# Optimization experiments

Hardware: AMD Instinct MI355X
Metric: run time of the kernel (lower is better)

Reference implementation:

```python
import jax, jax.numpy as jnp
import numpy as np

PD_THR = 1e-6  # positive-definiteness floor for the diagonal covariance

N_IN, DIM, BATCH = 8192, 128, 4096


def setup_inputs() -> dict:
    key = jax.random.key(0)
    kx, km = jax.random.split(key)
    x = jax.random.normal(kx, (BATCH, DIM), dtype=jnp.float32)
    mean = jax.random.normal(km, (N_IN, DIM), dtype=jnp.float32)
    diag = jnp.ones((N_IN, DIM), dtype=jnp.float32)
    return {"x": x, "mean": mean, "diag": diag}


def reference(x, mean, diag):
    """Energies[b, i] = KL( N(x_b, I) || N(mean_i, diag(diag_i)) ).

    Diagonal-Gaussian KL:
      0.5 * sum_d [ log(diag_id) + (1 + (x_bd - mu_id)^2) / diag_id - 1 ]

    The pairwise quadratic term is expanded into GEMMs to avoid the
    (batch, n_in, dim) broadcast intermediate:
      sum_d (x-mu)^2/diag = x^2 @ inv.T - 2 x @ (mu*inv).T + sum(mu^2*inv)
    Returns (batch, n_in), i.e. the original's energies.T.
    """
    d = jnp.clip(diag, PD_THR, None)              # (n_in, dim)
    inv = 1.0 / d                                 # (n_in, dim)
    # pairwise Mahalanobis quadratic, shape (batch, n_in)
    quad = (
        (x * x) @ inv.T
        - 2.0 * (x @ (mean * inv).T)
        + jnp.sum(mean * mean * inv, axis=-1)     # (n_in,) broadcast
    )
    # per-codebook constants: logdet + trace(inv) - dim
    const = jnp.sum(jnp.log(d), axis=-1) + jnp.sum(inv, axis=-1) - x.shape[-1]
    return 0.5 * (quad + const)                   # (batch, n_in)
```

## Files before the change

### kernel.cpp

```cpp
#include <hip/hip_runtime.h>
#include <hip/hip_bf16.h>


#define BATCH 4096
#define N_IN  8192
#define DIM   128
#define KPA   512
#define KPB   256
#define PD_THR 1e-6f

#define BM 256
#define BN 256
#define BK 64
#define NT (KPA / BK)

typedef __attribute__((ext_vector_type(4))) float f32x4;
typedef __attribute__((ext_vector_type(8))) short bf16x8;

static __device__ __forceinline__ unsigned short f2bf(float v) {
    union { __hip_bfloat16 h; unsigned short u; } cv;
    cv.h = __float2bfloat16(v);
    return cv.u;
}
static __device__ __forceinline__ float bf2f(unsigned short u) {
    union { unsigned short u; __hip_bfloat16 h; } cv;
    cv.u = u;
    return __bfloat162float(cv.h);
}

__global__ void prep_a_kernel(const float* __restrict__ x,
                              unsigned short* __restrict__ Ap) {
    int t = blockIdx.x * 256 + threadIdx.x;
    int row = t >> 7;
    int d   = t & 127;
    float v  = x[t];
    float x2 = v * v;
    unsigned short x2h = f2bf(x2);
    unsigned short x2l = f2bf(x2 - bf2f(x2h));
    unsigned short xh  = f2bf(v);
    unsigned short xl  = f2bf(v - bf2f(xh));
    unsigned short* a = Ap + (size_t)row * KPA;
    a[d]       = x2h;  a[128 + d] = xh;
    a[256 + d] = x2l;  a[384 + d] = xl;
}

__global__ void prep_b_kernel(const float* __restrict__ mean,
                              const float* __restrict__ diag,
                              unsigned short* __restrict__ Bp,
                              float* __restrict__ cvec) {
    int wave = threadIdx.x >> 6, lane = threadIdx.x & 63;
    int row = blockIdx.x * 4 + wave;
    const float* mrow = mean + (size_t)row * DIM;
    const float* drow = diag + (size_t)row * DIM;
    unsigned short* b = Bp + (size_t)row * KPB;
    float csum = 0.0f;
#pragma unroll
    for (int j = 0; j < 2; ++j) {
        int d = lane + 64 * j;
        float m   = mrow[d];
        float dd  = fmaxf(drow[d], PD_THR);
        float inv = 1.0f / dd;
        float fm  = -2.0f * m * inv;
        csum += m * m * inv + logf(dd) + inv;
        b[d]       = f2bf(inv);
        b[128 + d] = f2bf(fm);
    }
#pragma unroll
    for (int off = 32; off > 0; off >>= 1) csum += __shfl_down(csum, off);
    if (lane == 0) cvec[row] = csum - (float)DIM;
}

__global__ void __launch_bounds__(512, 2)
kl_gemm(const unsigned short* __restrict__ Ap,
        const unsigned short* __restrict__ Bp,
        const float* __restrict__ cvec,
        float* __restrict__ out) {
    __shared__ __align__(16) unsigned short lds[2][2 * BM * BK];

    int bid0 = blockIdx.x;
    int xcd = bid0 & 7, g = bid0 >> 3;
    int bx = (xcd & 1) * 8 + (g & 7);
    int by = (xcd >> 1) * 8 + (g >> 3);
    int m0 = bx * BM, n0 = by * BN;

    int tid  = threadIdx.x;
    int wave = tid >> 6, lane = tid & 63;
    int wr = wave >> 2, wc = wave & 3;

    const int lrow  = lane >> 3;
    const int lslot = (lane & 7) ^ lrow;

    const unsigned short* gA = Ap + (size_t)(m0 + wave * 8 + lrow) * KPA + lslot * 8;
    const unsigned short* gB = Bp + (size_t)(n0 + wave * 8 + lrow) * KPB + lslot * 8;

    f32x4 acc[8][4];
#pragma unroll
    for (int m = 0; m < 8; ++m)
#pragma unroll
        for (int n = 0; n < 4; ++n) acc[m][n] = (f32x4){0.f, 0.f, 0.f, 0.f};

    auto STAGE = [&](int b, int t) {
        int k0a = t * BK;
        int k0b = (t & 3) * BK;
#pragma unroll
        for (int j = 0; j < 4; ++j)
            __builtin_amdgcn_global_load_lds(
                (const __attribute__((address_space(1))) void*)(gA + (size_t)j * 64 * KPA + k0a),
                (__attribute__((address_space(3))) void*)&lds[b][(wave * 8 + j * 64) * 64],
                16, 0, 0);
#pragma unroll
        for (int j = 0; j < 4; ++j)
            __builtin_amdgcn_global_load_lds(
                (const __attribute__((address_space(1))) void*)(gB + (size_t)j * 64 * KPB + k0b),
                (__attribute__((address_space(3))) void*)&lds[b][16384 + (wave * 8 + j * 64) * 64],
                16, 0, 0);
    };

    auto COMPUTE = [&](int b) {
        const unsigned short* La = &lds[b][0];
        const unsigned short* Lb = &lds[b][16384];
#pragma unroll
        for (int kk = 0; kk < BK; kk += 32) {
            const int phys = ((((kk >> 3) + (lane >> 4))) ^ (lane & 7)) * 8;
            bf16x8 af[8], bf[4];
#pragma unroll
            for (int m = 0; m < 8; ++m)
                af[m] = *(const bf16x8*)&La[(wr * 128 + m * 16 + (lane & 15)) * 64 + phys];
#pragma unroll
            for (int n = 0; n < 4; ++n)
                bf[n] = *(const bf16x8*)&Lb[(wc * 64 + n * 16 + (lane & 15)) * 64 + phys];
            __builtin_amdgcn_s_setprio(1);
#pragma unroll
            for (int m = 0; m < 8; ++m)
#pragma unroll
                for (int n = 0; n < 4; ++n)
                    acc[m][n] = __builtin_amdgcn_mfma_f32_16x16x32_bf16(
                        af[m], bf[n], acc[m][n], 0, 0, 0);
            __builtin_amdgcn_s_setprio(0);
        }
    };

    STAGE(0, 0);
    STAGE(1, 1);
#pragma unroll 1
    for (int t = 0; t < NT - 1; ++t) {
        asm volatile("s_waitcnt vmcnt(8)" ::: "memory");
        __builtin_amdgcn_s_barrier();
        __builtin_amdgcn_sched_barrier(0);
        COMPUTE(t & 1);
        __builtin_amdgcn_s_barrier();
        __builtin_amdgcn_sched_barrier(0);
        if (t + 2 < NT) STAGE(t & 1, t + 2);
    }
    asm volatile("s_waitcnt vmcnt(0)" ::: "memory");
    __builtin_amdgcn_s_barrier();
    __builtin_amdgcn_sched_barrier(0);
    COMPUTE((NT - 1) & 1);
    __builtin_amdgcn_s_barrier();
    __builtin_amdgcn_sched_barrier(0);

    float* lbw = (float*)&lds[0][0] + wave * 1024;
    const int crow0 = m0 + wr * 128;
    const int ccol0 = n0 + wc * 64;
    const int lr = (lane >> 4) << 2;
    const int lc = lane & 15;
#pragma unroll
    for (int m = 0; m < 8; ++m) {
#pragma unroll
        for (int n = 0; n < 4; ++n)
#pragma unroll
            for (int r = 0; r < 4; ++r)
                lbw[(lr + r) * 64 + n * 16 + lc] = acc[m][n][r];
#pragma unroll
        for (int q = 0; q < 4; ++q) {
            int flat = q * 256 + lane * 4;
            int row  = flat >> 6;
            int col  = flat & 63;
            f32x4 v  = *(const f32x4*)&lbw[flat];
            f32x4 c4 = *(const f32x4*)&cvec[ccol0 + col];
            f32x4 o  = (v + c4) * 0.5f;
            __builtin_nontemporal_store(
                o, (f32x4*)&out[(size_t)(crow0 + m * 16 + row) * N_IN + ccol0 + col]);
        }
    }
}

extern "C" void kernel_launch(void* const* d_in, const int* in_sizes, int n_in_args,
                              void* d_out, int out_size, void* d_ws, size_t ws_size,
                              hipStream_t stream) {
    (void)in_sizes; (void)n_in_args; (void)out_size; (void)ws_size;
    const float* x    = (const float*)d_in[0];
    const float* mean = (const float*)d_in[1];
    const float* diag = (const float*)d_in[2];
    float* out = (float*)d_out;

    char* ws = (char*)d_ws;
    unsigned short* Bp = (unsigned short*)ws;
    unsigned short* Ap = (unsigned short*)(ws + (size_t)N_IN * KPB * 2);
    float* cvec = (float*)(ws + (size_t)N_IN * KPB * 2 + (size_t)BATCH * KPA * 2);

    prep_a_kernel<<<BATCH * DIM / 256, 256, 0, stream>>>(x, Ap);
    prep_b_kernel<<<N_IN / 4, 256, 0, stream>>>(mean, diag, Bp, cvec);
    kl_gemm<<<(BATCH / BM) * (N_IN / BN), 512, 0, stream>>>(Ap, Bp, cvec, out);
}
```

Before: 188.9 us.

## Shrink GEMM N tile to 128 and use triple-buffered LDS pipeline

Halves the block N tile from 256 to 128, so each wave computes a 64x64 sub-tile (4x4 MFMA accumulators instead of 8x4). LDS goes from two buffers to three, with loads issued three k-steps ahead and stepped vmcnt waits. The block-to-XCD mapping is reworked for the new 16x64 grid. This cuts register pressure and hides more global-load latency, but lowers arithmetic intensity per block and increases A-tile reloads across blocks.

```diff
diff --git a/kernel.cpp b/kernel.cpp
--- a/kernel.cpp
+++ b/kernel.cpp
@@ -10,9 +10,10 @@
 #define PD_THR 1e-6f
 
 #define BM 256
-#define BN 256
+#define BN 128
 #define BK 64
 #define NT (KPA / BK)
+#define BUFE (BM * BK + BN * BK)
 
 typedef __attribute__((ext_vector_type(4))) float f32x4;
 typedef __attribute__((ext_vector_type(8))) short bf16x8;
@@ -75,63 +76,64 @@
         const unsigned short* __restrict__ Bp,
         const float* __restrict__ cvec,
         float* __restrict__ out) {
-    __shared__ __align__(16) unsigned short lds[2][2 * BM * BK];
+    __shared__ __align__(16) unsigned short lds[3 * BUFE];
 
     int bid0 = blockIdx.x;
     int xcd = bid0 & 7, g = bid0 >> 3;
-    int bx = (xcd & 1) * 8 + (g & 7);
-    int by = (xcd >> 1) * 8 + (g >> 3);
+    int bx = (xcd & 3) * 4 + (g & 3);
+    int by = (xcd >> 2) * 32 + (g >> 2);
     int m0 = bx * BM, n0 = by * BN;
 
     int tid  = threadIdx.x;
     int wave = tid >> 6, lane = tid & 63;
-    int wr = wave >> 2, wc = wave & 3;
+    int wr = wave >> 1, wc = wave & 1;
 
     const int lrow  = lane >> 3;
     const int lslot = (lane & 7) ^ lrow;
 
     const unsigned short* gA = Ap + (size_t)(m0 + wave * 8 + lrow) * KPA + lslot * 8;
-    const unsigned short* gB = Bp + (size_t)(n0 + wave * 8 + lrow) * KPB + lslot * 8;
-
-    f32x4 acc[8][4];
-#pragma unroll
-    for (int m = 0; m < 8; ++m)
+    const unsigned short* gB = Bp + (size_t)(n0 + wave * 16 + lrow) * KPB + lslot * 8;
+
+    f32x4 acc[4][4];
+#pragma unroll
+    for (int m = 0; m < 4; ++m)
 #pragma unroll
         for (int n = 0; n < 4; ++n) acc[m][n] = (f32x4){0.f, 0.f, 0.f, 0.f};
 
     auto STAGE = [&](int b, int t) {
         int k0a = t * BK;
         int k0b = (t & 3) * BK;
+        unsigned short* base = &lds[b * BUFE];
 #pragma unroll
         for (int j = 0; j < 4; ++j)
             __builtin_amdgcn_global_load_lds(
                 (const __attribute__((address_space(1))) void*)(gA + (size_t)j * 64 * KPA + k0a),
-                (__attribute__((address_space(3))) void*)&lds[b][(wave * 8 + j * 64) * 64],
+                (__attribute__((address_space(3))) void*)&base[(wave * 8 + j * 64) * 64],
                 16, 0, 0);
 #pragma unroll
-        for (int j = 0; j < 4; ++j)
+        for (int j = 0; j < 2; ++j)
             __builtin_amdgcn_global_load_lds(
-                (const __attribute__((address_space(1))) void*)(gB + (size_t)j * 64 * KPB + k0b),
-                (__attribute__((address_space(3))) void*)&lds[b][16384 + (wave * 8 + j * 64) * 64],
+                (const __attribute__((address_space(1))) void*)(gB + (size_t)j * 8 * KPB + k0b),
+                (__attribute__((address_space(3))) void*)&base[BM * BK + (wave * 16 + j * 8) * 64],
                 16, 0, 0);
     };
 
     auto COMPUTE = [&](int b) {
-        const unsigned short* La = &lds[b][0];
-        const unsigned short* Lb = &lds[b][16384];
+        const unsigned short* La = &lds[b * BUFE];
+        const unsigned short* Lb = &lds[b * BUFE + BM * BK];
 #pragma unroll
         for (int kk = 0; kk < BK; kk += 32) {
-            const int phys = ((((kk >> 3) + (lane >> 4))) ^ (lane & 7)) * 8;
-            bf16x8 af[8], bf[4];
-#pragma unroll
-            for (int m = 0; m < 8; ++m)
-                af[m] = *(const bf16x8*)&La[(wr * 128 + m * 16 + (lane & 15)) * 64 + phys];
+            const int phys = (((kk >> 3) + (lane >> 4)) ^ (lane & 7)) * 8;
+            bf16x8 af[4], bf[4];
+#pragma unroll
+            for (int m = 0; m < 4; ++m)
+                af[m] = *(const bf16x8*)&La[(wr * 64 + m * 16 + (lane & 15)) * 64 + phys];
 #pragma unroll
             for (int n = 0; n < 4; ++n)
                 bf[n] = *(const bf16x8*)&Lb[(wc * 64 + n * 16 + (lane & 15)) * 64 + phys];
             __builtin_amdgcn_s_setprio(1);
 #pragma unroll
-            for (int m = 0; m < 8; ++m)
+            for (int m = 0; m < 4; ++m)
 #pragma unroll
                 for (int n = 0; n < 4; ++n)
                     acc[m][n] = __builtin_amdgcn_mfma_f32_16x16x32_bf16(
@@ -142,30 +144,29 @@
 
     STAGE(0, 0);
     STAGE(1, 1);
+    STAGE(2, 2);
+    int b = 0;
 #pragma unroll 1
-    for (int t = 0; t < NT - 1; ++t) {
-        asm volatile("s_waitcnt vmcnt(8)" ::: "memory");
+    for (int t = 0; t < NT; ++t) {
+        if (t < NT - 2)      asm volatile("s_waitcnt vmcnt(12)" ::: "memory");
+        else if (t == NT - 2) asm volatile("s_waitcnt vmcnt(6)"  ::: "memory");
+        else                  asm volatile("s_waitcnt vmcnt(0)"  ::: "memory");
         __builtin_amdgcn_s_barrier();
         __builtin_amdgcn_sched_barrier(0);
-        COMPUTE(t & 1);
+        COMPUTE(b);
         __builtin_amdgcn_s_barrier();
         __builtin_amdgcn_sched_barrier(0);
-        if (t + 2 < NT) STAGE(t & 1, t + 2);
+        if (t + 3 < NT) STAGE(b, t + 3);
+        b = (b == 2) ? 0 : b + 1;
     }
-    asm volatile("s_waitcnt vmcnt(0)" ::: "memory");
-    __builtin_amdgcn_s_barrier();
-    __builtin_amdgcn_sched_barrier(0);
-    COMPUTE((NT - 1) & 1);
-    __builtin_amdgcn_s_barrier();
-    __builtin_amdgcn_sched_barrier(0);
-
-    float* lbw = (float*)&lds[0][0] + wave * 1024;
-    const int crow0 = m0 + wr * 128;
+
+    float* lbw = (float*)&lds[0] + wave * 1024;
+    const int crow0 = m0 + wr * 64;
     const int ccol0 = n0 + wc * 64;
     const int lr = (lane >> 4) << 2;
     const int lc = lane & 15;
 #pragma unroll
-    for (int m = 0; m < 8; ++m) {
+    for (int m = 0; m < 4; ++m) {
 #pragma unroll
         for (int n = 0; n < 4; ++n)
 #pragma unroll
```

Result: no change. 189.2 us (+0.2%).

## Switch GEMM to 4-slot BK=32 ring buffer with deeper prefetch

Applied to the files above, without the earlier changes.

Replaces the double-buffered BK=64 pipeline with a four-slot ring of BK=32 sub-tiles, prefetching three stages ahead and issuing the next load right after the barrier, before the MFMAs of the current stage. The loop is fully unrolled with staged vmcnt waits, the LDS swizzle is reworked for the 32-wide rows, and the XCD-to-tile mapping is reshaped to 4x16. The aim is to hide global-to-LDS latency better and improve L2 locality, at the cost of more barriers per K and code size from the full unroll.

```diff
diff --git a/kernel.cpp b/kernel.cpp
--- a/kernel.cpp
+++ b/kernel.cpp
@@ -11,8 +11,8 @@
 
 #define BM 256
 #define BN 256
-#define BK 64
-#define NT (KPA / BK)
+#define NSUB 16
+#define SLOT 16384
 
 typedef __attribute__((ext_vector_type(4))) float f32x4;
 typedef __attribute__((ext_vector_type(8))) short bf16x8;
@@ -75,23 +75,22 @@
         const unsigned short* __restrict__ Bp,
         const float* __restrict__ cvec,
         float* __restrict__ out) {
-    __shared__ __align__(16) unsigned short lds[2][2 * BM * BK];
+    __shared__ __align__(16) unsigned short lds[4 * SLOT];
 
     int bid0 = blockIdx.x;
     int xcd = bid0 & 7, g = bid0 >> 3;
-    int bx = (xcd & 1) * 8 + (g & 7);
-    int by = (xcd >> 1) * 8 + (g >> 3);
+    int bx = (xcd & 3) * 4 + (g & 3);
+    int by = (xcd >> 2) * 16 + (g >> 2);
     int m0 = bx * BM, n0 = by * BN;
 
     int tid  = threadIdx.x;
     int wave = tid >> 6, lane = tid & 63;
     int wr = wave >> 2, wc = wave & 3;
 
-    const int lrow  = lane >> 3;
-    const int lslot = (lane & 7) ^ lrow;
-
-    const unsigned short* gA = Ap + (size_t)(m0 + wave * 8 + lrow) * KPA + lslot * 8;
-    const unsigned short* gB = Bp + (size_t)(n0 + wave * 8 + lrow) * KPB + lslot * 8;
+    const int srow  = lane >> 2;
+    const int sslot = (lane & 3) ^ ((lane >> 3) & 3);
+    const unsigned short* gA = Ap + (size_t)(m0 + wave * 16 + srow) * KPA + sslot * 8;
+    const unsigned short* gB = Bp + (size_t)(n0 + wave * 16 + srow) * KPB + sslot * 8;
 
     f32x4 acc[8][4];
 #pragma unroll
@@ -99,67 +98,59 @@
 #pragma unroll
         for (int n = 0; n < 4; ++n) acc[m][n] = (f32x4){0.f, 0.f, 0.f, 0.f};
 
-    auto STAGE = [&](int b, int t) {
-        int k0a = t * BK;
-        int k0b = (t & 3) * BK;
+    auto STAGE = [&](int s) {
+        unsigned short* base = &lds[(s & 3) * SLOT];
+        int ka = s * 32;
+        int kb = (s & 7) * 32;
 #pragma unroll
-        for (int j = 0; j < 4; ++j)
+        for (int j = 0; j < 2; ++j)
             __builtin_amdgcn_global_load_lds(
-                (const __attribute__((address_space(1))) void*)(gA + (size_t)j * 64 * KPA + k0a),
-                (__attribute__((address_space(3))) void*)&lds[b][(wave * 8 + j * 64) * 64],
+                (const __attribute__((address_space(1))) void*)(gA + (size_t)j * 128 * KPA + ka),
+                (__attribute__((address_space(3))) void*)&base[(j * 128 + wave * 16) * 32],
                 16, 0, 0);
 #pragma unroll
-        for (int j = 0; j < 4; ++j)
+        for (int j = 0; j < 2; ++j)
             __builtin_amdgcn_global_load_lds(
-                (const __attribute__((address_space(1))) void*)(gB + (size_t)j * 64 * KPB + k0b),
-                (__attribute__((address_space(3))) void*)&lds[b][16384 + (wave * 8 + j * 64) * 64],
+                (const __attribute__((address_space(1))) void*)(gB + (size_t)j * 128 * KPB + kb),
+                (__attribute__((address_space(3))) void*)&base[8192 + (j * 128 + wave * 16) * 32],
                 16, 0, 0);
     };
 
-    auto COMPUTE = [&](int b) {
-        const unsigned short* La = &lds[b][0];
-        const unsigned short* Lb = &lds[b][16384];
+    STAGE(0); STAGE(1); STAGE(2);
+
+    const int rphys = ((lane >> 4) ^ ((lane >> 1) & 3)) * 8;
+    const int l15   = lane & 15;
+
 #pragma unroll
-        for (int kk = 0; kk < BK; kk += 32) {
-            const int phys = ((((kk >> 3) + (lane >> 4))) ^ (lane & 7)) * 8;
-            bf16x8 af[8], bf[4];
+    for (int s = 0; s < NSUB; ++s) {
+        if (s <= 13)      asm volatile("s_waitcnt vmcnt(8)" ::: "memory");
+        else if (s == 14) asm volatile("s_waitcnt vmcnt(4)" ::: "memory");
+        else              asm volatile("s_waitcnt vmcnt(0)" ::: "memory");
+        __builtin_amdgcn_s_barrier();
+        __builtin_amdgcn_sched_barrier(0);
+        if (s + 3 < NSUB) STAGE(s + 3);
+        const unsigned short* La = &lds[(s & 3) * SLOT];
+        const unsigned short* Lb = La + 8192;
+        bf16x8 af[8], bf[4];
 #pragma unroll
-            for (int m = 0; m < 8; ++m)
-                af[m] = *(const bf16x8*)&La[(wr * 128 + m * 16 + (lane & 15)) * 64 + phys];
+        for (int m = 0; m < 8; ++m)
+            af[m] = *(const bf16x8*)&La[(wr * 128 + m * 16 + l15) * 32 + rphys];
+#pragma unroll
+        for (int n = 0; n < 4; ++n)
+            bf[n] = *(const bf16x8*)&Lb[(wc * 64 + n * 16 + l15) * 32 + rphys];
+        __builtin_amdgcn_s_setprio(1);
+#pragma unroll
+        for (int m = 0; m < 8; ++m)
 #pragma unroll
             for (int n = 0; n < 4; ++n)
-                bf[n] = *(const bf16x8*)&Lb[(wc * 64 + n * 16 + (lane & 15)) * 64 + phys];
-            __builtin_amdgcn_s_setprio(1);
-#pragma unroll
-            for (int m = 0; m < 8; ++m)
-#pragma unroll
-                for (int n = 0; n < 4; ++n)
-                    acc[m][n] = __builtin_amdgcn_mfma_f32_16x16x32_bf16(
-                        af[m], bf[n], acc[m][n], 0, 0, 0);
-            __builtin_amdgcn_s_setprio(0);
-        }
-    };
-
-    STAGE(0, 0);
-    STAGE(1, 1);
-#pragma unroll 1
-    for (int t = 0; t < NT - 1; ++t) {
-        asm volatile("s_waitcnt vmcnt(8)" ::: "memory");
+                acc[m][n] = __builtin_amdgcn_mfma_f32_16x16x32_bf16(
+                    af[m], bf[n], acc[m][n], 0, 0, 0);
+        __builtin_amdgcn_s_setprio(0);
         __builtin_amdgcn_s_barrier();
         __builtin_amdgcn_sched_barrier(0);
-        COMPUTE(t & 1);
-        __builtin_amdgcn_s_barrier();
-        __builtin_amdgcn_sched_barrier(0);
-        if (t + 2 < NT) STAGE(t & 1, t + 2);
     }
-    asm volatile("s_waitcnt vmcnt(0)" ::: "memory");
-    __builtin_amdgcn_s_barrier();
-    __builtin_amdgcn_sched_barrier(0);
-    COMPUTE((NT - 1) & 1);
-    __builtin_amdgcn_s_barrier();
-    __builtin_amdgcn_sched_barrier(0);
 
-    float* lbw = (float*)&lds[0][0] + wave * 1024;
+    float* lbw = (float*)&lds[0] + wave * 1024;
     const int crow0 = m0 + wr * 128;
     const int ccol0 = n0 + wc * 64;
     const int lr = (lane >> 4) << 2;
```

Measured after the change: 187.3 us. About the same (-0.9%).
